# Kernel tuning notes

Hardware: AMD Instinct MI355X
Metric: run time of the kernel (lower is better)

## Reference

```python
import jax, jax.numpy as jnp
import numpy as np

D = 256      # embed_dim
H = 2        # num_heads
DH = D // H  # head_dim = 128
NL = 4       # number of MHA layers
L = 4096     # num faces (queries)
S = 8192     # num edges (keys/values)
E_LOOP = 32  # edges per face loop


def setup_inputs() -> dict:
    key = jax.random.key(0)
    ks = jax.random.split(key, 8)
    v_face_edge_loop = jax.random.randint(ks[0], (L, E_LOOP), 0, S, dtype=jnp.int64)
    v_face_mask = jnp.ones((L,), dtype=bool)
    v_edge_embedding = jax.random.normal(ks[1], (S, D), dtype=jnp.float32)
    v_face_embedding = jax.random.normal(ks[2], (L, D), dtype=jnp.float32)
    # per-layer MHA params, stacked along a leading layer dim (PyTorch layout: W [out,in])
    sc = 1.0 / np.sqrt(D)
    in_proj_w = jax.random.normal(ks[3], (NL, 3 * D, D), dtype=jnp.float32) * sc
    in_proj_b = jnp.zeros((NL, 3 * D), dtype=jnp.float32)
    out_proj_w = jax.random.normal(ks[4], (NL, D, D), dtype=jnp.float32) * sc
    out_proj_b = jnp.zeros((NL, D), dtype=jnp.float32)
    return {
        "v_face_edge_loop": v_face_edge_loop,
        "v_face_mask": v_face_mask,
        "v_edge_embedding": v_edge_embedding,
        "v_face_embedding": v_face_embedding,
        "in_proj_w": in_proj_w,
        "in_proj_b": in_proj_b,
        "out_proj_w": out_proj_w,
        "out_proj_b": out_proj_b,
    }


def _build_mask(loop, face_mask, n_edges):
    # rows with face_mask==False contribute no scatter (mapped to sentinel col S, trimmed)
    rel = jnp.where(face_mask[:, None], loop, -1)
    valid = (rel != -1) & (rel != -2)
    rel = jnp.where(valid, rel, n_edges)  # invalid -> overflow column
    n_faces = loop.shape[0]
    m = jnp.zeros((n_faces, n_edges + 1), dtype=bool)
    m = m.at[jnp.arange(n_faces)[:, None], rel].set(True)
    return m[:, :n_edges]  # [L, S]; True = NOT allowed (PyTorch attn_mask semantics)


def _mha(x, kv, mask, wqkv, bqkv, wo, bo):
    wq, wk, wv = jnp.split(wqkv, 3, axis=0)
    bq, bk, bv = jnp.split(bqkv, 3, axis=0)
    q = (x @ wq.T + bq).reshape(-1, H, DH)    # [L,H,DH]
    k = (kv @ wk.T + bk).reshape(-1, H, DH)   # [S,H,DH]
    v = (kv @ wv.T + bv).reshape(-1, H, DH)   # [S,H,DH]
    scores = jnp.einsum('lhd,shd->hls', q, k) / np.float32(np.sqrt(DH))
    scores = jnp.where(mask[None, :, :], -jnp.inf, scores)
    attn = jax.nn.softmax(scores, axis=-1)
    out = jnp.einsum('hls,shd->lhd', attn, v).reshape(-1, D)
    return out @ wo.T + bo


def reference(v_face_edge_loop, v_face_mask, v_edge_embedding, v_face_embedding,
              in_proj_w, in_proj_b, out_proj_w, out_proj_b):
    n_edges = v_edge_embedding.shape[0]
    mask = _build_mask(v_face_edge_loop, v_face_mask, n_edges)
    x = v_face_embedding
    for i in range(NL):
        x = _mha(x, v_edge_embedding, mask,
                 in_proj_w[i], in_proj_b[i], out_proj_w[i], out_proj_b[i])
    return x
```

## Files before the change

kernel.cpp:

```cpp
#include <hip/hip_runtime.h>
#include <math.h>

typedef _Float16 f16;
typedef _Float16 f16x4 __attribute__((ext_vector_type(4)));
typedef _Float16 f16x8 __attribute__((ext_vector_type(8)));
typedef float f32x4 __attribute__((ext_vector_type(4)));
typedef float f32x16 __attribute__((ext_vector_type(16)));

#define MFMA_F16 __builtin_amdgcn_mfma_f32_16x16x32_f16
#define MFMA32_F16 __builtin_amdgcn_mfma_f32_32x32x16_f16

namespace {
constexpr int kL = 4096;
constexpr int kS = 8192;
constexpr int kD = 256;
constexpr int kH = 2;
constexpr int kDH = 128;
constexpr int kNL = 4;
constexpr int kNS = 8;
constexpr float kScale = 0.08838834764831845f;
}

__global__ __launch_bounds__(256) void cvt_all_k(
    const float* __restrict__ edge, const float* __restrict__ face,
    const float* __restrict__ inw, const float* __restrict__ outw,
    f16* __restrict__ e16, f16* __restrict__ xa,
    f16* __restrict__ win16, f16* __restrict__ wout16) {
  for (int i = blockIdx.x * 256 + threadIdx.x; i < 1048576; i += 1024 * 256) {
    const float* src;
    f16* dst;
    int off;
    if (i < 524288) { src = edge; dst = e16; off = i; }
    else if (i < 786432) { src = face; dst = xa; off = i - 524288; }
    else if (i < 983040) { src = inw; dst = win16; off = i - 786432; }
    else { src = outw; dst = wout16; off = i - 983040; }
    float4 v = *(const float4*)(src + 4 * (size_t)off);
    f16x4 h;
    h[0] = (f16)v.x; h[1] = (f16)v.y; h[2] = (f16)v.z; h[3] = (f16)v.w;
    *(f16x4*)(dst + 4 * (size_t)off) = h;
  }
}

__global__ __launch_bounds__(256) void detect_k(const unsigned int* __restrict__ loopw,
                                                const unsigned char* __restrict__ maskb,
                                                int* __restrict__ flags) {
  __shared__ unsigned int s[3];
  if (threadIdx.x < 3) s[threadIdx.x] = 0;
  __syncthreads();
  unsigned int orodd = 0;
  for (int i = 1 + 2 * threadIdx.x; i < 2048; i += 512) orodd |= loopw[i];
  unsigned int nz1 = 0, nz4 = 0;
  for (int i = threadIdx.x; i < 512; i += 256) {
    unsigned char b = maskb[i];
    if ((i & 3) != 0) nz1 |= b;
    if ((i & 7) == 4) nz4 |= b;
  }
  atomicOr(&s[0], orodd);
  atomicOr(&s[1], nz1);
  atomicOr(&s[2], nz4);
  __syncthreads();
  if (threadIdx.x == 0) {
    flags[0] = (s[0] == 0) ? 2 : 1;
    flags[1] = s[1] ? 1 : (s[2] ? 4 : 8);
  }
}

__device__ __forceinline__ void gemm_core(const f16* __restrict__ A,
                                          const f16* __restrict__ W, int K,
                                          int m0, int n0, int r, int g,
                                          f32x4 acc[2][2]) {
  const f16* ap0 = A + (size_t)(m0 + r) * K + g * 8;
  const f16* ap1 = ap0 + (size_t)16 * K;
  const f16* bp0 = W + (size_t)(n0 + r) * K + g * 8;
  const f16* bp1 = bp0 + (size_t)16 * K;
#pragma unroll 8
  for (int kc = 0; kc < K; kc += 32) {
    f16x8 a0 = *(const f16x8*)(ap0 + kc);
    f16x8 a1 = *(const f16x8*)(ap1 + kc);
    f16x8 b0 = *(const f16x8*)(bp0 + kc);
    f16x8 b1 = *(const f16x8*)(bp1 + kc);
    acc[0][0] = MFMA_F16(a0, b0, acc[0][0], 0, 0, 0);
    acc[0][1] = MFMA_F16(a0, b1, acc[0][1], 0, 0, 0);
    acc[1][0] = MFMA_F16(a1, b0, acc[1][0], 0, 0, 0);
    acc[1][1] = MFMA_F16(a1, b1, acc[1][1], 0, 0, 0);
  }
}

__global__ __launch_bounds__(256) void qkv_gemm_k(
    const f16* __restrict__ x, const f16* __restrict__ e16,
    const f16* __restrict__ wql, const float* __restrict__ biasl,
    f16* __restrict__ q16, f16* __restrict__ k16,
    f16* __restrict__ vt16, f16* __restrict__ v16) {
  const int lane = threadIdx.x & 63;
  const int wid = threadIdx.x >> 6;
  const int r = lane & 15, g = lane >> 4;
  const int bid = blockIdx.x;
  const bool qmode = bid < 256;
  int bx, by;
  const f16* A;
  const f16* W;
  const float* bias;
  if (qmode) {
    bx = bid & 63; by = bid >> 6;
    A = x; W = wql; bias = biasl;
  } else {
    int t = bid - 256;
    bx = t & 127; by = t >> 7;
    A = e16; W = wql + (size_t)kD * kD; bias = biasl + kD;
  }
  const int m0 = bx * 64 + (wid >> 1) * 32;
  const int n0 = by * 64 + (wid & 1) * 32;
  f32x4 acc[2][2] = {};
  gemm_core(A, W, kD, m0, n0, r, g, acc);

#pragma unroll
  for (int mt = 0; mt < 2; ++mt)
#pragma unroll
    for (int nt = 0; nt < 2; ++nt) {
      int col = n0 + nt * 16 + r;
      float bv = bias[col];
#pragma unroll
      for (int i = 0; i < 4; ++i) {
        int row = m0 + mt * 16 + g * 4 + i;
        float v = acc[mt][nt][i] + bv;
        if (qmode) {
          q16[(size_t)row * kD + col] = (f16)v;
        } else if (col < 256) {
          k16[(size_t)row * 256 + col] = (f16)v;
        } else {
          int dv = col - 256;
          vt16[(size_t)dv * kS + row] = (f16)v;
          v16[(size_t)row * 256 + dv] = (f16)v;
        }
      }
    }
}

__global__ __launch_bounds__(256) void gemm_awt_k(
    const f16* __restrict__ A, const f16* __restrict__ W,
    const float* __restrict__ bias, f16* __restrict__ C16,
    float* __restrict__ C32, int M, int N, int K) {
  const int lane = threadIdx.x & 63;
  const int wid = threadIdx.x >> 6;
  const int r = lane & 15, g = lane >> 4;
  const int m0 = blockIdx.x * 64 + (wid >> 1) * 32;
  const int n0 = blockIdx.y * 64 + (wid & 1) * 32;
  f32x4 acc[2][2] = {};
  gemm_core(A, W, K, m0, n0, r, g, acc);
#pragma unroll
  for (int mt = 0; mt < 2; ++mt)
#pragma unroll
    for (int nt = 0; nt < 2; ++nt) {
      int col = n0 + nt * 16 + r;
      float bv = bias[col];
#pragma unroll
      for (int i = 0; i < 4; ++i) {
        int row = m0 + mt * 16 + g * 4 + i;
        float v = acc[mt][nt][i] + bv;
        C16[(size_t)row * N + col] = (f16)v;
        if (C32) C32[(size_t)row * N + col] = v;
      }
    }
}

__device__ __forceinline__ unsigned pkh(float a, float b) {
  auto h2 = __builtin_amdgcn_cvt_pkrtz(a, b);
  return __builtin_bit_cast(unsigned, h2);
}
__device__ __forceinline__ void pswap(unsigned a, unsigned b, unsigned& x,
                                      unsigned& y) {
  typedef int i32x2 __attribute__((ext_vector_type(2)));
  i32x2 rr = __builtin_amdgcn_permlane32_swap((int)a, (int)b, false, false);
  x = (unsigned)rr[0];
  y = (unsigned)rr[1];
}
__device__ __forceinline__ f16x8 build_pfrag(float p0, float p1, float p2,
                                             float p3, float p4, float p5,
                                             float p6, float p7) {
  unsigned a0 = pkh(p0, p1), b0 = pkh(p4, p5);
  unsigned a1 = pkh(p2, p3), b1 = pkh(p6, p7);
  unsigned w0, w1, w2, w3;
  pswap(a0, b0, w0, w2);
  pswap(a1, b1, w1, w3);
  union { unsigned u[4]; f16x8 v; } r;
  r.u[0] = w0; r.u[1] = w1; r.u[2] = w2; r.u[3] = w3;
  return r.v;
}

__global__ __launch_bounds__(256, 2) void attn_dense3_k(
    const f16* __restrict__ Q, const f16* __restrict__ Km,
    const f16* __restrict__ Vt,
    f16* __restrict__ numOut, float* __restrict__ denOut) {
  __shared__ __align__(16) f16 Kl[2][64 * 128];
  __shared__ __align__(16) f16 Vl[2][128 * 64];
  const int tid = threadIdx.x;
  const int lane = tid & 63, wid = tid >> 6;
  const int la = lane & 31, hi = lane >> 5;
  const int h = blockIdx.y;
  const int q0w = blockIdx.x * 128 + wid * 32;
  const int sb0 = blockIdx.z * (kS / kNS);
  const int nt = (kS / kNS) / 64;

  f16x8 qb[8];
#pragma unroll
  for (int kk = 0; kk < 8; ++kk)
    qb[kk] = *(const f16x8*)(Q + (size_t)(q0w + la) * kD + h * kDH + kk * 16 +
                             hi * 8);

  int kSrc[4], kDst[4], vSrc[4], vDst[4];
#pragma unroll
  for (int p = 0; p < 4; ++p) {
    int m = wid * 16 + p * 4 + (lane >> 4);
    int s = lane & 15;
    kSrc[p] = (sb0 + m) * kD + h * kDH + 8 * (s ^ (m & 7));
    kDst[p] = m * 128 + 8 * s;
    int cv = p * 256 + tid;
    int d = cv >> 3, sv = cv & 7;
    vSrc[p] = (h * kDH + d) * kS + sb0 + 8 * (sv ^ (d & 7));
    vDst[p] = d * 64 + 8 * sv;
  }

  f32x16 o0 = {}, o1 = {}, o2 = {}, o3 = {};
  float den = 0.0f;
  f16x8 kst[4], vst[4];

#pragma unroll
  for (int p = 0; p < 4; ++p) {
    kst[p] = *(const f16x8*)(Km + kSrc[p]);
    vst[p] = *(const f16x8*)(Vt + vSrc[p]);
  }
#pragma unroll
  for (int p = 0; p < 4; ++p) {
    *(f16x8*)&Kl[0][kDst[p]] = kst[p];
    *(f16x8*)&Vl[0][vDst[p]] = vst[p];
  }
  __syncthreads();

  for (int t = 0; t < nt; ++t) {
    const int cur = t & 1;
    if (t + 1 < nt) {
#pragma unroll
      for (int p = 0; p < 4; ++p) {
        kst[p] = *(const f16x8*)(Km + kSrc[p] + (t + 1) * 64 * kD);
        vst[p] = *(const f16x8*)(Vt + vSrc[p] + (t + 1) * 64);
      }
    }

    f32x16 st0 = {}, st1 = {};
#pragma unroll
    for (int kk = 0; kk < 8; ++kk) {
      int sl = 8 * ((kk * 2 + hi) ^ (la & 7));
      f16x8 k0 = *(const f16x8*)&Kl[cur][la * 128 + sl];
      f16x8 k1 = *(const f16x8*)&Kl[cur][(32 + la) * 128 + sl];
      st0 = MFMA32_F16(k0, qb[kk], st0, 0, 0, 0);
      st1 = MFMA32_F16(k1, qb[kk], st1, 0, 0, 0);
    }

    f32x16 pe0, pe1;
#pragma unroll
    for (int i = 0; i < 16; ++i) {
      pe0[i] = __expf(st0[i] * kScale);
      pe1[i] = __expf(st1[i] * kScale);
    }
#pragma unroll
    for (int i = 0; i < 16; ++i) den += pe0[i] + pe1[i];

    f16x8 pf[4];
    pf[0] = build_pfrag(pe0[0], pe0[1], pe0[2], pe0[3], pe0[4], pe0[5], pe0[6], pe0[7]);
    pf[1] = build_pfrag(pe0[8], pe0[9], pe0[10], pe0[11], pe0[12], pe0[13], pe0[14], pe0[15]);
    pf[2] = build_pfrag(pe1[0], pe1[1], pe1[2], pe1[3], pe1[4], pe1[5], pe1[6], pe1[7]);
    pf[3] = build_pfrag(pe1[8], pe1[9], pe1[10], pe1[11], pe1[12], pe1[13], pe1[14], pe1[15]);

#pragma unroll
    for (int dt = 0; dt < 4; ++dt) {
      int d = dt * 32 + la;
      f32x16* op = (dt == 0) ? &o0 : (dt == 1) ? &o1 : (dt == 2) ? &o2 : &o3;
#pragma unroll
      for (int ks = 0; ks < 4; ++ks) {
        f16x8 vf = *(const f16x8*)&Vl[cur][d * 64 + 8 * ((ks * 2 + hi) ^ (d & 7))];
        *op = MFMA32_F16(vf, pf[ks], *op, 0, 0, 0);
      }
    }

    if (t + 1 < nt) {
      const int nxt = cur ^ 1;
#pragma unroll
      for (int p = 0; p < 4; ++p) {
        *(f16x8*)&Kl[nxt][kDst[p]] = kst[p];
        *(f16x8*)&Vl[nxt][vDst[p]] = vst[p];
      }
      __syncthreads();
    }
  }

  const size_t base = ((size_t)blockIdx.z * kH + h) * kL + q0w;
#pragma unroll
  for (int dt = 0; dt < 4; ++dt) {
    const f32x16* op = (dt == 0) ? &o0 : (dt == 1) ? &o1 : (dt == 2) ? &o2 : &o3;
#pragma unroll
    for (int gq = 0; gq < 4; ++gq) {
      int d0 = dt * 32 + gq * 8 + 4 * hi;
      f16x4 w;
      w[0] = (f16)(*op)[4 * gq + 0];
      w[1] = (f16)(*op)[4 * gq + 1];
      w[2] = (f16)(*op)[4 * gq + 2];
      w[3] = (f16)(*op)[4 * gq + 3];
      *(f16x4*)&numOut[(base + la) * kDH + d0] = w;
    }
  }
  float dq = den + __shfl_xor(den, 32);
  if (lane < 32) denOut[base + lane] = dq;
}

__global__ __launch_bounds__(256) void corrcomb_k(
    const unsigned int* __restrict__ loopw, const unsigned char* __restrict__ maskb,
    const int* __restrict__ flags,
    const f16* __restrict__ Q, const f16* __restrict__ Km,
    const f16* __restrict__ V,
    const f16* __restrict__ numb, const float* __restrict__ denb,
    f16* __restrict__ out16) {
  __shared__ float cvL[4][128];
  __shared__ float csL[4];
  const int lane = threadIdx.x & 63;
  const int wid = threadIdx.x >> 6;
  const int w = blockIdx.x * 4 + wid;
  const int f = w >> 1, h = w & 1;
  const int lstride = flags[0];
  const int mstride = flags[1];

  int idx = -1, valid = 0;
  if (lane < 32) {
    idx = (int)loopw[(size_t)(f * 32 + lane) * lstride];
    valid = maskb[(size_t)f * mstride] ? 1 : 0;
  }
#pragma unroll
  for (int j = 0; j < 32; ++j) {
    int oidx = __shfl(idx, j);
    if (lane < 32 && j < lane && oidx == idx) valid = 0;
  }

  const size_t qb = (size_t)f * kD + h * kDH + 2 * lane;
  const float qa = (float)Q[qb];
  const float qbv = (float)Q[qb + 1];
  float s0 = 0.0f, cv0 = 0.0f, cv1 = 0.0f;
  for (int e = 0; e < 32; ++e) {
    int ei = __shfl(idx, e);
    int ev = __shfl(valid, e);
    if (!ev) continue;
    size_t kb = (size_t)ei * kD + h * kDH + 2 * lane;
    float part = qa * (float)Km[kb] + qbv * (float)Km[kb + 1];
#pragma unroll
    for (int m = 1; m < 64; m <<= 1) part += __shfl_xor(part, m);
    float pe = __expf(part * kScale);
    s0 += pe;
    cv0 += pe * (float)V[kb];
    cv1 += pe * (float)V[kb + 1];
  }
  cvL[wid][2 * lane] = cv0;
  cvL[wid][2 * lane + 1] = cv1;
  if (lane == 0) csL[wid] = s0;
  __syncthreads();

#pragma unroll
  for (int e = 0; e < 2; ++e) {
    int idx2 = e * 256 + threadIdx.x;
    int floc = idx2 >> 8;
    int c = idx2 & 255;
    int h2 = c >> 7;
    int d = c & 127;
    int widx = floc * 2 + h2;
    int fabs_ = blockIdx.x * 2 + floc;
    float n = -cvL[widx][d];
    float dn = -csL[widx];
#pragma unroll
    for (int z = 0; z < kNS; ++z) {
      n += (float)numb[((size_t)(z * kH + h2) * kL + fabs_) * kDH + d];
      dn += denb[(size_t)(z * kH + h2) * kL + fabs_];
    }
    out16[(size_t)fabs_ * kD + h2 * kDH + d] = (f16)(n / dn);
  }
}

extern "C" void kernel_launch(void* const* d_in, const int* in_sizes, int n_in,
                              void* d_out, int out_size, void* d_ws, size_t ws_size,
                              hipStream_t stream) {
  const unsigned int* loopw = (const unsigned int*)d_in[0];
  const unsigned char* fmask = (const unsigned char*)d_in[1];
  const float* edge = (const float*)d_in[2];
  const float* face = (const float*)d_in[3];
  const float* inw = (const float*)d_in[4];
  const float* inb = (const float*)d_in[5];
  const float* outw = (const float*)d_in[6];
  const float* outb = (const float*)d_in[7];
  float* out = (float*)d_out;

  char* p = (char*)d_ws;
  auto alloc = [&](size_t bytes) {
    char* q = p;
    p += (bytes + 255) & ~(size_t)255;
    return q;
  };
  int* flags = (int*)alloc(256);
  f16* e16 = (f16*)alloc((size_t)kS * kD * 2);
  f16* win16 = (f16*)alloc((size_t)kNL * 3 * kD * kD * 2);
  f16* wout16 = (f16*)alloc((size_t)kNL * kD * kD * 2);
  f16* xa = (f16*)alloc((size_t)kL * kD * 2);
  f16* xb = (f16*)alloc((size_t)kL * kD * 2);
  f16* q16 = (f16*)alloc((size_t)kL * kD * 2);
  f16* k16 = (f16*)alloc((size_t)kS * kD * 2);
  f16* v16 = (f16*)alloc((size_t)kS * kD * 2);
  f16* vt16 = (f16*)alloc((size_t)kS * kD * 2);
  f16* ao16 = (f16*)alloc((size_t)kL * kD * 2);
  f16* numb = (f16*)alloc((size_t)kNS * kH * kL * kDH * 2);
  float* denb = (float*)alloc((size_t)kNS * kH * kL * 4);

  detect_k<<<1, 256, 0, stream>>>(loopw, fmask, flags);
  cvt_all_k<<<1024, 256, 0, stream>>>(edge, face, inw, outw, e16, xa, win16,
                                      wout16);

  f16* x = xa;
  f16* xn = xb;
  for (int l = 0; l < kNL; ++l) {
    const f16* wql = win16 + (size_t)l * 3 * kD * kD;
    qkv_gemm_k<<<1280, 256, 0, stream>>>(x, e16, wql, inb + l * 3 * kD, q16,
                                         k16, vt16, v16);
    attn_dense3_k<<<dim3(kL / 128, kH, kNS), 256, 0, stream>>>(q16, k16, vt16,
                                                               numb, denb);
    corrcomb_k<<<kL / 2, 256, 0, stream>>>(loopw, fmask, flags, q16, k16, v16,
                                           numb, denb, ao16);
    gemm_awt_k<<<dim3(kL / 64, kD / 64), 256, 0, stream>>>(
        ao16, wout16 + (size_t)l * kD * kD, outb + l * kD, xn,
        (l == kNL - 1) ? out : nullptr, kL, kD, kD);
    f16* tmp = x;
    x = xn;
    xn = tmp;
  }
}
```

Measured before the change: 434.4 us.

## Stream K/V directly from global in attention, double key splits, tile V transpose

The attention kernel stops staging K and V tiles through double-buffered LDS with barriers and loads MFMA fragments straight from global memory (relying on cache). It raises occupancy to 3 blocks per CU, brackets the MFMA loops with s_setprio, and doubles the key-split count to 16. The V transpose in the QKV GEMM now goes through an LDS tile so that the vt16 writes are coalesced. The numerator partials are stored transposed ([d][L]), and the combine kernel is updated to read that layout. The risks are uncoalesced, uncached global fragment loads, and twice as much partial-sum traffic in the combine step.

```diff
diff --git a/kernel.cpp b/kernel.cpp
--- a/kernel.cpp
+++ b/kernel.cpp
@@ -17,7 +17,7 @@
 constexpr int kH = 2;
 constexpr int kDH = 128;
 constexpr int kNL = 4;
-constexpr int kNS = 8;
+constexpr int kNS = 16;
 constexpr float kScale = 0.08838834764831845f;
 }
 
@@ -91,6 +91,7 @@
     const f16* __restrict__ wql, const float* __restrict__ biasl,
     f16* __restrict__ q16, f16* __restrict__ k16,
     f16* __restrict__ vt16, f16* __restrict__ v16) {
+  __shared__ __align__(16) f16 Tl[64][72];
   const int lane = threadIdx.x & 63;
   const int wid = threadIdx.x >> 6;
   const int r = lane & 15, g = lane >> 4;
@@ -110,6 +111,7 @@
   }
   const int m0 = bx * 64 + (wid >> 1) * 32;
   const int n0 = by * 64 + (wid & 1) * 32;
+  const bool vmode = !qmode && (by >= 4);
   f32x4 acc[2][2] = {};
   gemm_core(A, W, kD, m0, n0, r, g, acc);
 
@@ -125,15 +127,29 @@
         float v = acc[mt][nt][i] + bv;
         if (qmode) {
           q16[(size_t)row * kD + col] = (f16)v;
-        } else if (col < 256) {
+        } else if (!vmode) {
           k16[(size_t)row * 256 + col] = (f16)v;
         } else {
           int dv = col - 256;
-          vt16[(size_t)dv * kS + row] = (f16)v;
           v16[(size_t)row * 256 + dv] = (f16)v;
+          int nl = (wid & 1) * 32 + nt * 16 + r;
+          int rl = (wid >> 1) * 32 + mt * 16 + g * 4 + i;
+          Tl[nl][rl] = (f16)v;
         }
       }
     }
+  if (vmode) {
+    __syncthreads();
+    const int dvb = (by - 4) * 64;
+    const int key0 = bx * 64;
+#pragma unroll
+    for (int it = 0; it < 2; ++it) {
+      int rowd = it * 32 + (threadIdx.x >> 3);
+      int seg = (threadIdx.x & 7) * 8;
+      *(f16x8*)&vt16[(size_t)(dvb + rowd) * kS + key0 + seg] =
+          *(const f16x8*)&Tl[rowd][seg];
+    }
+  }
 }
 
 __global__ __launch_bounds__(256) void gemm_awt_k(
@@ -187,14 +203,11 @@
   return r.v;
 }
 
-__global__ __launch_bounds__(256, 2) void attn_dense3_k(
+__global__ __launch_bounds__(256, 3) void attn_dense4_k(
     const f16* __restrict__ Q, const f16* __restrict__ Km,
     const f16* __restrict__ Vt,
-    f16* __restrict__ numOut, float* __restrict__ denOut) {
-  __shared__ __align__(16) f16 Kl[2][64 * 128];
-  __shared__ __align__(16) f16 Vl[2][128 * 64];
-  const int tid = threadIdx.x;
-  const int lane = tid & 63, wid = tid >> 6;
+    f16* __restrict__ numT, float* __restrict__ denOut) {
+  const int lane = threadIdx.x & 63, wid = threadIdx.x >> 6;
   const int la = lane & 31, hi = lane >> 5;
   const int h = blockIdx.y;
   const int q0w = blockIdx.x * 128 + wid * 32;
@@ -207,54 +220,24 @@
     qb[kk] = *(const f16x8*)(Q + (size_t)(q0w + la) * kD + h * kDH + kk * 16 +
                              hi * 8);
 
-  int kSrc[4], kDst[4], vSrc[4], vDst[4];
-#pragma unroll
-  for (int p = 0; p < 4; ++p) {
-    int m = wid * 16 + p * 4 + (lane >> 4);
-    int s = lane & 15;
-    kSrc[p] = (sb0 + m) * kD + h * kDH + 8 * (s ^ (m & 7));
-    kDst[p] = m * 128 + 8 * s;
-    int cv = p * 256 + tid;
-    int d = cv >> 3, sv = cv & 7;
-    vSrc[p] = (h * kDH + d) * kS + sb0 + 8 * (sv ^ (d & 7));
-    vDst[p] = d * 64 + 8 * sv;
-  }
-
   f32x16 o0 = {}, o1 = {}, o2 = {}, o3 = {};
   float den = 0.0f;
-  f16x8 kst[4], vst[4];
-
-#pragma unroll
-  for (int p = 0; p < 4; ++p) {
-    kst[p] = *(const f16x8*)(Km + kSrc[p]);
-    vst[p] = *(const f16x8*)(Vt + vSrc[p]);
-  }
-#pragma unroll
-  for (int p = 0; p < 4; ++p) {
-    *(f16x8*)&Kl[0][kDst[p]] = kst[p];
-    *(f16x8*)&Vl[0][vDst[p]] = vst[p];
-  }
-  __syncthreads();
+
+  const f16* kb = Km + (size_t)sb0 * kD + h * kDH + hi * 8;
+  const f16* vb = Vt + (size_t)(h * kDH) * kS + sb0 + hi * 8;
 
   for (int t = 0; t < nt; ++t) {
-    const int cur = t & 1;
-    if (t + 1 < nt) {
-#pragma unroll
-      for (int p = 0; p < 4; ++p) {
-        kst[p] = *(const f16x8*)(Km + kSrc[p] + (t + 1) * 64 * kD);
-        vst[p] = *(const f16x8*)(Vt + vSrc[p] + (t + 1) * 64);
-      }
-    }
-
+    const f16* kt = kb + (size_t)t * 64 * kD;
     f32x16 st0 = {}, st1 = {};
+    __builtin_amdgcn_s_setprio(1);
 #pragma unroll
     for (int kk = 0; kk < 8; ++kk) {
-      int sl = 8 * ((kk * 2 + hi) ^ (la & 7));
-      f16x8 k0 = *(const f16x8*)&Kl[cur][la * 128 + sl];
-      f16x8 k1 = *(const f16x8*)&Kl[cur][(32 + la) * 128 + sl];
+      f16x8 k0 = *(const f16x8*)(kt + (size_t)la * kD + kk * 16);
+      f16x8 k1 = *(const f16x8*)(kt + (size_t)(32 + la) * kD + kk * 16);
       st0 = MFMA32_F16(k0, qb[kk], st0, 0, 0, 0);
       st1 = MFMA32_F16(k1, qb[kk], st1, 0, 0, 0);
     }
+    __builtin_amdgcn_s_setprio(0);
 
     f32x16 pe0, pe1;
 #pragma unroll
@@ -271,45 +254,35 @@
     pf[2] = build_pfrag(pe1[0], pe1[1], pe1[2], pe1[3], pe1[4], pe1[5], pe1[6], pe1[7]);
     pf[3] = build_pfrag(pe1[8], pe1[9], pe1[10], pe1[11], pe1[12], pe1[13], pe1[14], pe1[15]);
 
+    const f16* vt = vb + t * 64;
+    __builtin_amdgcn_s_setprio(1);
 #pragma unroll
     for (int dt = 0; dt < 4; ++dt) {
-      int d = dt * 32 + la;
       f32x16* op = (dt == 0) ? &o0 : (dt == 1) ? &o1 : (dt == 2) ? &o2 : &o3;
 #pragma unroll
       for (int ks = 0; ks < 4; ++ks) {
-        f16x8 vf = *(const f16x8*)&Vl[cur][d * 64 + 8 * ((ks * 2 + hi) ^ (d & 7))];
+        f16x8 vf = *(const f16x8*)(vt + (size_t)(dt * 32 + la) * kS + ks * 16);
         *op = MFMA32_F16(vf, pf[ks], *op, 0, 0, 0);
       }
     }
-
-    if (t + 1 < nt) {
-      const int nxt = cur ^ 1;
-#pragma unroll
-      for (int p = 0; p < 4; ++p) {
-        *(f16x8*)&Kl[nxt][kDst[p]] = kst[p];
-        *(f16x8*)&Vl[nxt][vDst[p]] = vst[p];
-      }
-      __syncthreads();
-    }
-  }
-
-  const size_t base = ((size_t)blockIdx.z * kH + h) * kL + q0w;
+    __builtin_amdgcn_s_setprio(0);
+  }
+
+  const size_t nbase = ((size_t)blockIdx.z * kH + h) * kDH * kL;
 #pragma unroll
   for (int dt = 0; dt < 4; ++dt) {
     const f32x16* op = (dt == 0) ? &o0 : (dt == 1) ? &o1 : (dt == 2) ? &o2 : &o3;
 #pragma unroll
-    for (int gq = 0; gq < 4; ++gq) {
-      int d0 = dt * 32 + gq * 8 + 4 * hi;
-      f16x4 w;
-      w[0] = (f16)(*op)[4 * gq + 0];
-      w[1] = (f16)(*op)[4 * gq + 1];
-      w[2] = (f16)(*op)[4 * gq + 2];
-      w[3] = (f16)(*op)[4 * gq + 3];
-      *(f16x4*)&numOut[(base + la) * kDH + d0] = w;
-    }
+    for (int gq = 0; gq < 4; ++gq)
+#pragma unroll
+      for (int i = 0; i < 4; ++i) {
+        int d = dt * 32 + gq * 8 + 4 * hi + i;
+        numT[nbase + (size_t)d * kL + q0w + la] = (f16)(*op)[4 * gq + i];
+      }
   }
   float dq = den + __shfl_xor(den, 32);
-  if (lane < 32) denOut[base + lane] = dq;
+  if (lane < 32)
+    denOut[((size_t)blockIdx.z * kH + h) * kL + q0w + lane] = dq;
 }
 
 __global__ __launch_bounds__(256) void corrcomb_k(
@@ -317,7 +290,7 @@
     const int* __restrict__ flags,
     const f16* __restrict__ Q, const f16* __restrict__ Km,
     const f16* __restrict__ V,
-    const f16* __restrict__ numb, const float* __restrict__ denb,
+    const f16* __restrict__ numT, const float* __restrict__ denb,
     f16* __restrict__ out16) {
   __shared__ float cvL[4][128];
   __shared__ float csL[4];
@@ -374,8 +347,8 @@
     float dn = -csL[widx];
 #pragma unroll
     for (int z = 0; z < kNS; ++z) {
-      n += (float)numb[((size_t)(z * kH + h2) * kL + fabs_) * kDH + d];
-      dn += denb[(size_t)(z * kH + h2) * kL + fabs_];
+      n += (float)numT[(((size_t)z * kH + h2) * kDH + d) * kL + fabs_];
+      dn += denb[((size_t)z * kH + h2) * kL + fabs_];
     }
     out16[(size_t)fabs_ * kD + h2 * kDH + d] = (f16)(n / dn);
   }
@@ -411,7 +384,7 @@
   f16* v16 = (f16*)alloc((size_t)kS * kD * 2);
   f16* vt16 = (f16*)alloc((size_t)kS * kD * 2);
   f16* ao16 = (f16*)alloc((size_t)kL * kD * 2);
-  f16* numb = (f16*)alloc((size_t)kNS * kH * kL * kDH * 2);
+  f16* numb = (f16*)alloc((size_t)kNS * kH * kDH * kL * 2);
   float* denb = (float*)alloc((size_t)kNS * kH * kL * 4);
 
   detect_k<<<1, 256, 0, stream>>>(loopw, fmask, flags);
@@ -424,7 +397,7 @@
     const f16* wql = win16 + (size_t)l * 3 * kD * kD;
     qkv_gemm_k<<<1280, 256, 0, stream>>>(x, e16, wql, inb + l * 3 * kD, q16,
                                          k16, vt16, v16);
-    attn_dense3_k<<<dim3(kL / 128, kH, kNS), 256, 0, stream>>>(q16, k16, vt16,
+    attn_dense4_k<<<dim3(kL / 128, kH, kNS), 256, 0, stream>>>(q16, k16, vt16,
                                                                numb, denb);
     corrcomb_k<<<kL / 2, 256, 0, stream>>>(loopw, fmask, flags, q16, k16, v16,
                                            numb, denb, ao16);
```

After: 1.246 ms. 2.87x slower.
